# Kernel optimization log

Measured on AMD Instinct MI355X. Metric: run time of the kernel, lower is better.

Reference implementation:

```python
import jax, jax.numpy as jnp
import numpy as np


def setup_inputs() -> dict:
    key = jax.random.key(0)
    k0, k1, k2, k3 = jax.random.split(key, 4)
    T, B, K, L, DEG = 2000, 2048, 64, 64, 3
    return {
        "currents": jax.random.normal(k0, (T, B), dtype=jnp.float32),
        "a": jax.random.normal(k1, (K,), dtype=jnp.float32) * 0.05,
        "b_lag": jax.random.normal(k2, (L,), dtype=jnp.float32) * 1e-3,
        "poly_coeff": jax.random.normal(k3, (1, DEG + 1), dtype=jnp.float32) * 0.3,
        "b_act": jnp.zeros((1,), dtype=jnp.float32),
        "max_current": jnp.full((1,), 100.0, dtype=jnp.float32),
        "max_firing_rate": jnp.full((1,), 100.0, dtype=jnp.float32),
    }


def _poly_act(z, poly_coeff, b_act, max_current, max_firing_rate):
    # PolynomialActivation.forward: x=(z-b)/max_current; poly=sum_d x^d * coeff_d^2
    x = (z - b_act[0]) / max_current[0]  # [B]
    deg = poly_coeff.shape[1] - 1
    coeff = (poly_coeff ** 2)[0]  # [deg+1]
    # build integer powers safely (negative bases) via repeated multiply
    pows = [jnp.ones_like(x)]
    for _ in range(deg):
        pows.append(pows[-1] * x)
    powers = jnp.stack(pows, axis=-1)  # [B, deg+1]
    poly = powers @ coeff  # [B]
    return jax.nn.relu(max_firing_rate[0] * jnp.tanh(poly))


def reference(currents, a, b_lag, poly_coeff, b_act, max_current, max_firing_rate):
    T, B = currents.shape
    K, L = a.shape[0], b_lag.shape[0]

    def step(carry, c_t):
        cur_buf, fs_buf = carry  # [B,K], [B,L]
        cur_buf = jnp.concatenate([cur_buf[:, 1:], c_t[:, None]], axis=1)
        x = cur_buf @ a                      # einsum('j,ij->i')
        y = 1000.0 * (fs_buf @ b_lag)        # einsum('j,ij->i')
        f = _poly_act(x + y, poly_coeff, b_act, max_current, max_firing_rate)
        fs_buf = jnp.concatenate([fs_buf[:, 1:], f[:, None]], axis=1)
        return (cur_buf, fs_buf), f

    init = (jnp.zeros((B, K), currents.dtype), jnp.zeros((B, L), currents.dtype))
    _, fs = jax.lax.scan(step, init, currents)  # fs: [T, B]
    return fs
```

## Files before the change

### kernel.cpp

```cpp
#include <hip/hip_runtime.h>

#define T_STEPS 2000
#define BATCH   2048
#define TPAD    2048
#define TT      16

__global__ __launch_bounds__(256) void conv_kernel(
    const float* __restrict__ currents, const float* __restrict__ a,
    const float* __restrict__ b_act, const float* __restrict__ max_current,
    float* __restrict__ xt)
{
    __shared__ float sa[64];
    int tid = threadIdx.x;
    if (tid < 64) sa[tid] = a[tid];
    __syncthreads();

    int b  = blockIdx.y * 256 + tid;
    int t0 = blockIdx.x * TT;

    float w[TT + 63];
#pragma unroll
    for (int k = 0; k < TT + 63; ++k) {
        int tau = t0 - 63 + k;
        w[k] = (tau >= 0 && tau < T_STEPS) ? currents[(long)tau * BATCH + b] : 0.0f;
    }

    float acc[TT];
#pragma unroll
    for (int i = 0; i < TT; ++i) acc[i] = 0.0f;

#pragma unroll
    for (int j = 0; j < 64; ++j) {
        float aj = sa[j];
#pragma unroll
        for (int i = 0; i < TT; ++i)
            acc[i] = fmaf(aj, w[i + j], acc[i]);
    }

    float ba     = b_act[0];
    float inv_mc = 1.0f / max_current[0];
#pragma unroll
    for (int i = 0; i < TT; ++i) {
        int t = t0 + i;
        if (t < T_STEPS) xt[(long)b * TPAD + t] = (acc[i] - ba) * inv_mc;
    }
}

__global__ __launch_bounds__(256) void recur_kernel(
    const float* __restrict__ xt, const float* __restrict__ b_lag,
    const float* __restrict__ poly_coeff, const float* __restrict__ max_current,
    const float* __restrict__ max_firing_rate, float* __restrict__ out)
{
    __shared__ float g2[128];
    int tid = threadIdx.x;
    float mc    = max_current[0];
    float scale = 1000.0f / mc;
    if (tid < 128) {
        int i = tid & 63;
        g2[tid] = scale * b_lag[63 - i];
    }
    __syncthreads();

    int lane = tid & 63;
    int wid  = tid >> 6;
    int b    = blockIdx.x * 4 + wid;

    const float K2 = 2.8853900817779268f;
    float c0 = poly_coeff[0], c1 = poly_coeff[1], c2 = poly_coeff[2], c3 = poly_coeff[3];
    float k0 = K2 * c0 * c0, k1 = K2 * c1 * c1, k2 = K2 * c2 * c2, k3 = K2 * c3 * c3;
    float M  = max_firing_rate[0];
    float m2 = -2.0f * M;

    float cf[64];
#pragma unroll
    for (int s = 0; s < 64; ++s) cf[s] = g2[lane + 63 - s];

    const float* xrow = xt + (long)b * TPAD;
    float acc = xrow[lane];
    float xn  = xrow[64 + lane];
    float fv  = 0.0f;
    float* outcol = out + b;

    auto step = [&](int s, float xcur) {
        float u = __builtin_bit_cast(float,
                    __builtin_amdgcn_readlane(__builtin_bit_cast(int, acc), s));
        float u2 = u * u;
        float a1 = fmaf(u, k1, k0);
        float a2 = fmaf(u, k3, k2);
        float p  = fminf(fmaf(u2, a2, a1), 126.0f);
        float e  = __builtin_amdgcn_exp2f(p);
        float r  = __builtin_amdgcn_rcpf(e + 1.0f);
        float f  = fmaxf(fmaf(m2, r, M), 0.0f);
        bool own = (lane == s);
        acc = fmaf(cf[s], f, own ? xcur : acc);
        fv  = own ? f : fv;
    };

    for (int chunk = 0; chunk < 31; ++chunk) {
        int t0  = chunk * 64;
        int tn2 = t0 + 128 + lane;
        float xn_next = (tn2 < T_STEPS) ? xrow[tn2] : 0.0f;
#pragma unroll
        for (int s = 0; s < 64; ++s) step(s, xn);
        outcol[(long)(t0 + lane) * BATCH] = fv;
        xn = xn_next;
    }
#pragma unroll
    for (int s = 0; s < 16; ++s) step(s, 0.0f);
    if (lane < 16) outcol[(long)(1984 + lane) * BATCH] = fv;
}

extern "C" void kernel_launch(void* const* d_in, const int* in_sizes, int n_in,
                              void* d_out, int out_size, void* d_ws, size_t ws_size,
                              hipStream_t stream) {
    const float* currents   = (const float*)d_in[0];
    const float* a          = (const float*)d_in[1];
    const float* b_lag      = (const float*)d_in[2];
    const float* poly_coeff = (const float*)d_in[3];
    const float* b_act      = (const float*)d_in[4];
    const float* mc         = (const float*)d_in[5];
    const float* mfr        = (const float*)d_in[6];
    float* out = (float*)d_out;
    float* xt  = (float*)d_ws;

    conv_kernel<<<dim3(T_STEPS / TT, BATCH / 256), 256, 0, stream>>>(
        currents, a, b_act, mc, xt);
    recur_kernel<<<BATCH / 4, 256, 0, stream>>>(
        xt, b_lag, poly_coeff, mc, mfr, out);
}
```

Baseline: 253.3 us.

## Fuse convolution into recurrence using a DPP-rotated pipelined accumulator

Merges the separate convolution and recurrence kernels into one. Each wave keeps a 64-lane running accumulator that holds partial sums for future time steps. Every step adds the broadcast current times a reversed weight, reads lane 0, then rotates by one lane with DPP and adds the feedback term. This drops the workspace round-trip for xt, one kernel launch, and the 64-entry per-lane coefficient array. In exchange each step gets longer because of an extra readlane, a DPP rotate and a select on the serial path, and the clamp on the exp argument is removed.

```diff
diff --git a/kernel.cpp b/kernel.cpp
--- a/kernel.cpp
+++ b/kernel.cpp
@@ -2,68 +2,22 @@
 
 #define T_STEPS 2000
 #define BATCH   2048
-#define TPAD    2048
-#define TT      16
 
-__global__ __launch_bounds__(256) void conv_kernel(
+__global__ __launch_bounds__(256) void fused_kernel(
     const float* __restrict__ currents, const float* __restrict__ a,
+    const float* __restrict__ b_lag, const float* __restrict__ poly_coeff,
     const float* __restrict__ b_act, const float* __restrict__ max_current,
-    float* __restrict__ xt)
-{
-    __shared__ float sa[64];
-    int tid = threadIdx.x;
-    if (tid < 64) sa[tid] = a[tid];
-    __syncthreads();
-
-    int b  = blockIdx.y * 256 + tid;
-    int t0 = blockIdx.x * TT;
-
-    float w[TT + 63];
-#pragma unroll
-    for (int k = 0; k < TT + 63; ++k) {
-        int tau = t0 - 63 + k;
-        w[k] = (tau >= 0 && tau < T_STEPS) ? currents[(long)tau * BATCH + b] : 0.0f;
-    }
-
-    float acc[TT];
-#pragma unroll
-    for (int i = 0; i < TT; ++i) acc[i] = 0.0f;
-
-#pragma unroll
-    for (int j = 0; j < 64; ++j) {
-        float aj = sa[j];
-#pragma unroll
-        for (int i = 0; i < TT; ++i)
-            acc[i] = fmaf(aj, w[i + j], acc[i]);
-    }
-
-    float ba     = b_act[0];
-    float inv_mc = 1.0f / max_current[0];
-#pragma unroll
-    for (int i = 0; i < TT; ++i) {
-        int t = t0 + i;
-        if (t < T_STEPS) xt[(long)b * TPAD + t] = (acc[i] - ba) * inv_mc;
-    }
-}
-
-__global__ __launch_bounds__(256) void recur_kernel(
-    const float* __restrict__ xt, const float* __restrict__ b_lag,
-    const float* __restrict__ poly_coeff, const float* __restrict__ max_current,
     const float* __restrict__ max_firing_rate, float* __restrict__ out)
 {
-    __shared__ float g2[128];
-    int tid = threadIdx.x;
-    float mc    = max_current[0];
-    float scale = 1000.0f / mc;
-    if (tid < 128) {
-        int i = tid & 63;
-        g2[tid] = scale * b_lag[63 - i];
-    }
-    __syncthreads();
-
+    int tid  = threadIdx.x;
     int lane = tid & 63;
     int wid  = tid >> 6;
     int b    = blockIdx.x * 4 + wid;
+
+    float inv = 1.0f / max_current[0];
+    float cba = -b_act[0] * inv;
+    float af  = a[63 - lane] * inv;
+    float gam = (1000.0f * inv) * b_lag[63 - lane];
 
     const float K2 = 2.8853900817779268f;
     float c0 = poly_coeff[0], c1 = poly_coeff[1], c2 = poly_coeff[2], c3 = poly_coeff[3];
@@ -71,42 +25,51 @@
     float M  = max_firing_rate[0];
     float m2 = -2.0f * M;
 
-    float cf[64];
-#pragma unroll
-    for (int s = 0; s < 64; ++s) cf[s] = g2[lane + 63 - s];
+    auto bcast = [](float v, int l) {
+        return __builtin_bit_cast(float,
+            __builtin_amdgcn_readlane(__builtin_bit_cast(int, v), l));
+    };
+    auto rotl1 = [](float v) {
+        int i = __builtin_bit_cast(int, v);
+        return __builtin_bit_cast(float,
+            __builtin_amdgcn_update_dpp(i, i, 0x134, 0xf, 0xf, false));
+    };
 
-    const float* xrow = xt + (long)b * TPAD;
-    float acc = xrow[lane];
-    float xn  = xrow[64 + lane];
-    float fv  = 0.0f;
-    float* outcol = out + b;
+    const float* ccol   = currents + b;
+    float*       outcol = out + b;
 
-    auto step = [&](int s, float xcur) {
-        float u = __builtin_bit_cast(float,
-                    __builtin_amdgcn_readlane(__builtin_bit_cast(int, acc), s));
+    float R  = cba;
+    float cv = ccol[(long)lane * BATCH];
+    float fv = 0.0f;
+
+    auto step = [&](int s) {
+        float c = bcast(cv, s);
+        R = fmaf(af, c, R);
+        float u = bcast(R, 0);
         float u2 = u * u;
         float a1 = fmaf(u, k1, k0);
         float a2 = fmaf(u, k3, k2);
-        float p  = fminf(fmaf(u2, a2, a1), 126.0f);
+        float p  = fmaf(u2, a2, a1);
         float e  = __builtin_amdgcn_exp2f(p);
         float r  = __builtin_amdgcn_rcpf(e + 1.0f);
         float f  = fmaxf(fmaf(m2, r, M), 0.0f);
-        bool own = (lane == s);
-        acc = fmaf(cf[s], f, own ? xcur : acc);
-        fv  = own ? f : fv;
+        float Rr = rotl1(R);
+        Rr = (lane == 63) ? cba : Rr;
+        R  = fmaf(gam, f, Rr);
+        fv = (lane == s) ? f : fv;
     };
 
     for (int chunk = 0; chunk < 31; ++chunk) {
-        int t0  = chunk * 64;
-        int tn2 = t0 + 128 + lane;
-        float xn_next = (tn2 < T_STEPS) ? xrow[tn2] : 0.0f;
+        int t0 = chunk * 64;
+        int tp = t0 + 64 + lane;
+        float cv_next = (tp < T_STEPS) ? ccol[(long)tp * BATCH] : 0.0f;
 #pragma unroll
-        for (int s = 0; s < 64; ++s) step(s, xn);
+        for (int s = 0; s < 64; ++s) step(s);
         outcol[(long)(t0 + lane) * BATCH] = fv;
-        xn = xn_next;
+        cv = cv_next;
     }
 #pragma unroll
-    for (int s = 0; s < 16; ++s) step(s, 0.0f);
+    for (int s = 0; s < 16; ++s) step(s);
     if (lane < 16) outcol[(long)(1984 + lane) * BATCH] = fv;
 }
 
@@ -121,10 +84,7 @@
     const float* mc         = (const float*)d_in[5];
     const float* mfr        = (const float*)d_in[6];
     float* out = (float*)d_out;
-    float* xt  = (float*)d_ws;
 
-    conv_kernel<<<dim3(T_STEPS / TT, BATCH / 256), 256, 0, stream>>>(
-        currents, a, b_act, mc, xt);
-    recur_kernel<<<BATCH / 4, 256, 0, stream>>>(
-        xt, b_lag, poly_coeff, mc, mfr, out);
+    fused_kernel<<<BATCH / 4, 256, 0, stream>>>(
+        currents, a, b_lag, poly_coeff, b_act, mc, mfr, out);
 }
```

After: 211.2 us. 1.2x faster.
